# Kernel optimization log

Hardware: AMD Instinct MI355X
Metric: run time of the kernel (lower is better)

Reference implementation:

```python
import jax, jax.numpy as jnp
import numpy as np

N = 100000        # nodes
E = 1600000       # edges (avg degree 16)
D_IN = 128        # input feature dim
LAT = [32, 32, 32]
HID = 128
G = 1000          # graphs in batch


def _glorot(k, shape):
    lim = float(np.sqrt(6.0 / (shape[0] + shape[1])))
    return jax.random.uniform(k, shape, jnp.float32, -lim, lim)


def setup_inputs() -> dict:
    key = jax.random.key(0)
    ks = jax.random.split(key, 8)
    x = jax.random.normal(ks[0], (N, D_IN), jnp.float32)
    edge_index = jax.random.randint(ks[1], (2, E), 0, N, jnp.int32)
    # sorted graph assignment, every graph non-empty
    batch = ((jnp.arange(N, dtype=jnp.int32) * G) // N).astype(jnp.int32)
    W1 = _glorot(ks[2], (D_IN, LAT[0]));  b1 = jnp.zeros((LAT[0],), jnp.float32)
    W2 = _glorot(ks[3], (LAT[0], LAT[1])); b2 = jnp.zeros((LAT[1],), jnp.float32)
    W3 = _glorot(ks[4], (LAT[1], LAT[2])); b3 = jnp.zeros((LAT[2],), jnp.float32)
    lin1_w = _glorot(ks[5], (sum(LAT), HID)); lin1_b = jnp.zeros((HID,), jnp.float32)
    lin2_w = _glorot(ks[6], (HID, 2));        lin2_b = jnp.zeros((2,), jnp.float32)
    return dict(x=x, edge_index=edge_index, batch=batch, num_graphs=G,
                W1=W1, b1=b1, W2=W2, b2=b2, W3=W3, b3=b3,
                lin1_w=lin1_w, lin1_b=lin1_b, lin2_w=lin2_w, lin2_b=lin2_b)


def reference(x, edge_index, batch, num_graphs,
              W1, b1, W2, b2, W3, b3, lin1_w, lin1_b, lin2_w, lin2_b):
    n = x.shape[0]
    src, dst = edge_index[0], edge_index[1]
    # GCN sym-normalization with self-loops: deg[i] = 1 + in-degree(i)
    deg = jnp.ones((n,), x.dtype).at[dst].add(1.0)
    dis = jax.lax.rsqrt(deg)                      # deg^{-1/2}
    coef = (dis[src] * dis[dst])[:, None]         # [E,1] edge norm
    self_coef = (dis * dis)[:, None]              # [N,1] self-loop norm

    def gcn(h, W, b):
        h = h @ W                                  # transform first (PyG order)
        agg = jax.ops.segment_sum(h[src] * coef, dst, num_segments=n)
        return agg + h * self_coef + b

    h1 = jnp.tanh(gcn(x,  W1, b1))
    h2 = jnp.tanh(gcn(h1, W2, b2))
    h3 = jnp.tanh(gcn(h2, W3, b3))
    cat = jnp.concatenate([h1, h2, h3], axis=1)    # [N, 96]
    # readout: first node of each graph (batch is sorted)
    idx = jnp.searchsorted(batch, jnp.arange(num_graphs, dtype=batch.dtype))
    g = cat[idx]                                   # [G, 96]
    hidden = jax.nn.relu(g @ lin1_w + lin1_b)
    logits = jax.nn.log_softmax(hidden @ lin2_w + lin2_b, axis=1)
    return logits
```

## Files before the change

kernel.cpp:

```cpp
#include <hip/hip_runtime.h>
#include <math.h>


typedef int      int4v   __attribute__((ext_vector_type(4)));
typedef float    float4v __attribute__((ext_vector_type(4)));
typedef _Float16 half4v  __attribute__((ext_vector_type(4)));

#define NBLK 256
#define SB   500
#define CAPE 10240

__global__ void k_hist(const int* __restrict__ dst, int* __restrict__ blk_hist,
                       int E, int NP) {
    __shared__ int h[256];
    for (int i = threadIdx.x; i < NP; i += 256) h[i] = 0;
    __syncthreads();
    const int4v* d4 = (const int4v*)dst;
    int nv = E >> 2;
    int stride = gridDim.x * blockDim.x;
    for (int i = blockIdx.x * blockDim.x + threadIdx.x; i < nv; i += stride) {
        int4v d = __builtin_nontemporal_load(&d4[i]);
#pragma unroll
        for (int j = 0; j < 4; ++j) atomicAdd(&h[d[j] / SB], 1);
    }
    if (blockIdx.x == 0) {
        for (int e = (nv << 2) + threadIdx.x; e < E; e += blockDim.x)
            atomicAdd(&h[dst[e] / SB], 1);
    }
    __syncthreads();
    for (int i = threadIdx.x; i < NP; i += 256)
        blk_hist[blockIdx.x * NP + i] = h[i];
}

__global__ void k_total(const int* __restrict__ blk_hist, int* __restrict__ total, int NP) {
    __shared__ int s[256];
    int f = blockIdx.x;
    int acc = 0;
    for (int b = threadIdx.x; b < NBLK; b += 256) acc += blk_hist[b * NP + f];
    s[threadIdx.x] = acc;
    __syncthreads();
    for (int off = 128; off > 0; off >>= 1) {
        if (threadIdx.x < off) s[threadIdx.x] += s[threadIdx.x + off];
        __syncthreads();
    }
    if (threadIdx.x == 0) total[f] = s[0];
}

__global__ void k_sbase(const int* __restrict__ total, int* __restrict__ sbase, int NP) {
    __shared__ int s[256];
    int t = threadIdx.x;
    int v = (t < NP) ? total[t] : 0;
    s[t] = v;
    __syncthreads();
    for (int off = 1; off < 256; off <<= 1) {
        int u = (t >= off) ? s[t - off] : 0;
        __syncthreads();
        s[t] += u;
        __syncthreads();
    }
    if (t < NP) sbase[t] = s[t] - v;
    if (t == NP - 1) sbase[NP] = s[t];
}

__global__ void k_binoff(const int* __restrict__ blk_hist, const int* __restrict__ sbase,
                         int* __restrict__ blk_off, int NP) {
    __shared__ int s[NBLK];
    int f = blockIdx.x;
    int b = threadIdx.x;
    int v = blk_hist[b * NP + f];
    s[b] = v;
    __syncthreads();
    for (int off = 1; off < NBLK; off <<= 1) {
        int u = (b >= off) ? s[b - off] : 0;
        __syncthreads();
        s[b] += u;
        __syncthreads();
    }
    blk_off[b * NP + f] = sbase[f] + s[b] - v;
}

__global__ void k_split(const int* __restrict__ src, const int* __restrict__ dst,
                        const int* __restrict__ blk_off, uint2* __restrict__ pairs,
                        int E, int NP) {
    __shared__ int goff[256];
    for (int f = threadIdx.x; f < NP; f += 256)
        goff[f] = blk_off[blockIdx.x * NP + f];
    __syncthreads();
    const int4v* d4 = (const int4v*)dst;
    const int4v* s4 = (const int4v*)src;
    int nv = E >> 2;
    int stride = gridDim.x * blockDim.x;
    for (int i = blockIdx.x * blockDim.x + threadIdx.x; i < nv; i += stride) {
        int4v d = __builtin_nontemporal_load(&d4[i]);
        int4v s = __builtin_nontemporal_load(&s4[i]);
#pragma unroll
        for (int j = 0; j < 4; ++j) {
            int f = d[j] / SB;
            int pos = atomicAdd(&goff[f], 1);
            pairs[pos] = make_uint2((unsigned)s[j], (unsigned)d[j]);
        }
    }
    if (blockIdx.x == 0) {
        for (int e = (nv << 2) + threadIdx.x; e < E; e += blockDim.x) {
            int f = dst[e] / SB;
            int pos = atomicAdd(&goff[f], 1);
            pairs[pos] = make_uint2((unsigned)src[e], (unsigned)dst[e]);
        }
    }
}

__global__ void __launch_bounds__(512)
k_place(const uint2* __restrict__ pairs, const int* __restrict__ sbase,
        int* __restrict__ rowptr, float* __restrict__ dis,
        int* __restrict__ csr_src, int N, int NP) {
    __shared__ int lcnt[SB];
    __shared__ int lrp[SB + 1];
    __shared__ int sc[512];
    __shared__ int stage[CAPE];
    int f = blockIdx.x;
    int lo = f * SB;
    if (lo >= N) return;
    int hi = lo + SB; if (hi > N) hi = N;
    int sbc = hi - lo;
    int p0 = sbase[f], p1 = sbase[f + 1];
    int base = p0;
    int tid = threadIdx.x;
    for (int i = tid; i < sbc; i += 512) lcnt[i] = 0;
    __syncthreads();
    {
        int i = p0 + tid;
        for (; i + 3 * 512 < p1; i += 4 * 512) {
            uint2 a = pairs[i], c = pairs[i + 512], d = pairs[i + 1024], e = pairs[i + 1536];
            unsigned la = a.y - lo, lc = c.y - lo, ld = d.y - lo, le = e.y - lo;
            if (la < (unsigned)sbc) atomicAdd(&lcnt[la], 1);
            if (lc < (unsigned)sbc) atomicAdd(&lcnt[lc], 1);
            if (ld < (unsigned)sbc) atomicAdd(&lcnt[ld], 1);
            if (le < (unsigned)sbc) atomicAdd(&lcnt[le], 1);
        }
        for (; i < p1; i += 512) {
            unsigned ly = pairs[i].y - lo;
            if (ly < (unsigned)sbc) atomicAdd(&lcnt[ly], 1);
        }
    }
    __syncthreads();
    for (int i = tid; i < sbc; i += 512) dis[lo + i] = rsqrtf(1.0f + (float)lcnt[i]);
    int v = (tid < sbc) ? lcnt[tid] : 0;
    sc[tid] = v;
    __syncthreads();
    for (int off = 1; off < 512; off <<= 1) {
        int u = (tid >= off) ? sc[tid - off] : 0;
        __syncthreads();
        sc[tid] += u;
        __syncthreads();
    }
    if (tid < sbc) lrp[tid] = sc[tid] - v;
    if (tid == 511) lrp[sbc] = sc[511];
    __syncthreads();
    int T = lrp[sbc];
    for (int i = tid; i < sbc; i += 512) rowptr[lo + i] = base + lrp[i];
    if (hi == N && tid == 0) rowptr[N] = base + T;
    for (int i = tid; i < sbc; i += 512) lcnt[i] = 0;
    __syncthreads();
    {
        int i = p0 + tid;
        for (; i + 3 * 512 < p1; i += 4 * 512) {
            uint2 a = pairs[i], c = pairs[i + 512], d = pairs[i + 1024], e = pairs[i + 1536];
#pragma unroll
            for (int j = 0; j < 4; ++j) {
                uint2 p = (j == 0) ? a : (j == 1) ? c : (j == 2) ? d : e;
                unsigned ly = p.y - lo;
                if (ly < (unsigned)sbc) {
                    int slot = lrp[ly] + atomicAdd(&lcnt[ly], 1);
                    if (T <= CAPE) stage[slot] = (int)p.x;
                    else           csr_src[base + slot] = (int)p.x;
                }
            }
        }
        for (; i < p1; i += 512) {
            uint2 p = pairs[i];
            unsigned ly = p.y - lo;
            if (ly < (unsigned)sbc) {
                int slot = lrp[ly] + atomicAdd(&lcnt[ly], 1);
                if (T <= CAPE) stage[slot] = (int)p.x;
                else           csr_src[base + slot] = (int)p.x;
            }
        }
    }
    __syncthreads();
    if (T <= CAPE)
        for (int j = tid; j < T; j += 512) csr_src[base + j] = stage[j];
}

__global__ void k_gemm1(const float* __restrict__ h, const float* __restrict__ W,
                        const float* __restrict__ dis, _Float16* __restrict__ hps, int n) {
    __shared__ float sW[128 * 32];
    __shared__ float sh[64 * 132];
    int tid = threadIdx.x;
    int row0 = blockIdx.x * 64;
    for (int j = tid; j < 1024; j += 128)
        *(float4*)&sW[j * 4] = *(const float4*)&W[j * 4];
    for (int j = tid; j < 2048; j += 128) {
        int r = j >> 5, c4 = j & 31;
        float4v v = {0.f, 0.f, 0.f, 0.f};
        if (row0 + r < n)
            v = __builtin_nontemporal_load((const float4v*)&h[(size_t)(row0 + r) * 128 + c4 * 4]);
        *(float4v*)&sh[r * 132 + c4 * 4] = v;
    }
    __syncthreads();
    int rg = tid >> 3;
    int cg = tid & 7;
    float acc[4][4] = {};
    const float* shp = &sh[(rg * 4) * 132];
    const float* swp = &sW[cg * 4];
#pragma unroll 8
    for (int k4 = 0; k4 < 32; ++k4) {
        float4 hv[4], wv[4];
#pragma unroll
        for (int r = 0; r < 4; ++r) hv[r] = *(const float4*)&shp[r * 132 + k4 * 4];
#pragma unroll
        for (int t = 0; t < 4; ++t) wv[t] = *(const float4*)&swp[(k4 * 4 + t) * 32];
#pragma unroll
        for (int r = 0; r < 4; ++r) {
            const float hr[4] = {hv[r].x, hv[r].y, hv[r].z, hv[r].w};
#pragma unroll
            for (int t = 0; t < 4; ++t) {
                acc[r][0] += hr[t] * wv[t].x;
                acc[r][1] += hr[t] * wv[t].y;
                acc[r][2] += hr[t] * wv[t].z;
                acc[r][3] += hr[t] * wv[t].w;
            }
        }
    }
#pragma unroll
    for (int r = 0; r < 4; ++r) {
        int row = row0 + rg * 4 + r;
        if (row < n) {
            float dv = dis[row];
            half4v o = { (_Float16)(acc[r][0] * dv), (_Float16)(acc[r][1] * dv),
                         (_Float16)(acc[r][2] * dv), (_Float16)(acc[r][3] * dv) };
            *(half4v*)&hps[(size_t)row * 32 + cg * 4] = o;
        }
    }
}

template <bool FUSE>
__global__ void k_agg(const _Float16* __restrict__ hps, const int* __restrict__ rowptr,
                      const int* __restrict__ csr_src, const float* __restrict__ dis,
                      const float* __restrict__ bias, float* __restrict__ outc,
                      int n, const float* __restrict__ Wn, _Float16* __restrict__ hpsn) {
    __shared__ float sW[32 * 32];
    if (FUSE) {
        for (int i = threadIdx.x; i < 1024; i += 256) sW[i] = Wn[i];
        __syncthreads();
    }
    int g    = (blockIdx.x * blockDim.x + threadIdx.x) >> 5;
    int lane = threadIdx.x & 31;
    if (g >= n) return;
    float acc = (float)hps[(size_t)g * 32 + lane];
    int e0 = rowptr[g], e1 = rowptr[g + 1];
    int e = e0;
    while (e < e1) {
        int m = e1 - e; if (m > 32) m = 32;
        int sv = (e + lane < e1) ? __builtin_nontemporal_load(&csr_src[e + lane]) : 0;
        int k = 0;
        for (; k + 8 <= m; k += 8) {
            float v[8];
#pragma unroll
            for (int j = 0; j < 8; ++j) {
                int s = __shfl(sv, k + j, 32);
                v[j] = (float)hps[(size_t)s * 32 + lane];
            }
            acc += ((v[0] + v[1]) + (v[2] + v[3])) + ((v[4] + v[5]) + (v[6] + v[7]));
        }
        if (k + 4 <= m) {
            float v[4];
#pragma unroll
            for (int j = 0; j < 4; ++j) {
                int s = __shfl(sv, k + j, 32);
                v[j] = (float)hps[(size_t)s * 32 + lane];
            }
            acc += (v[0] + v[1]) + (v[2] + v[3]);
            k += 4;
        }
        for (; k < m; ++k) {
            int s = __shfl(sv, k, 32);
            acc += (float)hps[(size_t)s * 32 + lane];
        }
        e += m;
    }
    float dg = dis[g];
    float v = tanhf(dg * acc + bias[lane]);
    __builtin_nontemporal_store(v, &outc[(size_t)g * 96 + lane]);
    if (FUSE) {
        float a2 = 0.0f;
#pragma unroll
        for (int k = 0; k < 32; ++k)
            a2 += __shfl(v, k, 32) * sW[k * 32 + lane];
        hpsn[(size_t)g * 32 + lane] = (_Float16)(dg * a2);
    }
}

__global__ void k_idx(const int* __restrict__ batch, int* __restrict__ idx, int n, int g) {
    int i = blockIdx.x * blockDim.x + threadIdx.x;
    if (i >= g) return;
    int lo = 0, hi = n;
    while (lo < hi) {
        int mid = (lo + hi) >> 1;
        if (batch[mid] < i) lo = mid + 1; else hi = mid;
    }
    idx[i] = lo;
}

__global__ void k_head(const float* __restrict__ cat, const int* __restrict__ idx,
                       const float* __restrict__ w1, const float* __restrict__ b1,
                       const float* __restrict__ w2, const float* __restrict__ b2,
                       float* __restrict__ out) {
    __shared__ float gv[96];
    __shared__ float s0[128];
    __shared__ float s1[128];
    int g = blockIdx.x, t = threadIdx.x;
    int node = idx[g];
    if (t < 96) gv[t] = cat[(size_t)node * 96 + t];
    __syncthreads();
    float acc = b1[t];
#pragma unroll 8
    for (int i = 0; i < 96; ++i) acc += gv[i] * w1[i * 128 + t];
    float h = fmaxf(acc, 0.0f);
    s0[t] = h * w2[t * 2 + 0];
    s1[t] = h * w2[t * 2 + 1];
    __syncthreads();
    for (int off = 64; off > 0; off >>= 1) {
        if (t < off) { s0[t] += s0[t + off]; s1[t] += s1[t + off]; }
        __syncthreads();
    }
    if (t == 0) {
        float l0 = s0[0] + b2[0];
        float l1 = s1[0] + b2[1];
        float m  = fmaxf(l0, l1);
        float lse = m + logf(expf(l0 - m) + expf(l1 - m));
        out[(size_t)g * 2 + 0] = l0 - lse;
        out[(size_t)g * 2 + 1] = l1 - lse;
    }
}

extern "C" void kernel_launch(void* const* d_in, const int* in_sizes, int n_in,
                              void* d_out, int out_size, void* d_ws, size_t ws_size,
                              hipStream_t stream) {
    const float* x    = (const float*)d_in[0];
    const int*   ei   = (const int*)d_in[1];
    const int*   batch= (const int*)d_in[2];
    const float* W1   = (const float*)d_in[4];
    const float* b1   = (const float*)d_in[5];
    const float* W2   = (const float*)d_in[6];
    const float* b2   = (const float*)d_in[7];
    const float* W3   = (const float*)d_in[8];
    const float* b3   = (const float*)d_in[9];
    const float* l1w  = (const float*)d_in[10];
    const float* l1b  = (const float*)d_in[11];
    const float* l2w  = (const float*)d_in[12];
    const float* l2b  = (const float*)d_in[13];
    float* out = (float*)d_out;

    const int N = in_sizes[0] / 128;
    const int E = in_sizes[1] / 2;
    const int G = out_size / 2;
    const int* src = ei;
    const int* dst = ei + E;

    const int NP = (N + SB - 1) / SB;

    char* w = (char*)d_ws;
    auto alloc = [&](size_t bytes) {
        char* p = w;
        w += (bytes + 255) & ~(size_t)255;
        return p;
    };
    float*    dis      = (float*)   alloc((size_t)N * 4);
    int*      rowptr   = (int*)     alloc((size_t)(N + 1) * 4);
    int*      csr_src  = (int*)     alloc((size_t)E * 4);
    int*      blk_hist = (int*)     alloc((size_t)NBLK * NP * 4);
    int*      total    = (int*)     alloc((size_t)NP * 4);
    int*      sbase    = (int*)     alloc((size_t)(NP + 1) * 4);
    int*      blk_off  = (int*)     alloc((size_t)NBLK * NP * 4);
    uint2*    pairs    = (uint2*)   alloc((size_t)E * 8);
    _Float16* hpsA     = (_Float16*)alloc((size_t)N * 32 * 2);
    _Float16* hpsB     = (_Float16*)alloc((size_t)N * 32 * 2);
    float*    catb     = (float*)   alloc((size_t)N * 96 * 4);
    int*      idx      = (int*)     alloc((size_t)G * 4);

    const int nodes_bl = (N * 32 + 255) / 256;
    const int gemm_bl  = (N + 63) / 64;

    k_hist  <<<NBLK, 256, 0, stream>>>(dst, blk_hist, E, NP);
    k_total <<<NP,   256, 0, stream>>>(blk_hist, total, NP);
    k_sbase <<<1,    256, 0, stream>>>(total, sbase, NP);
    k_binoff<<<NP,  NBLK, 0, stream>>>(blk_hist, sbase, blk_off, NP);
    k_split <<<NBLK, 256, 0, stream>>>(src, dst, blk_off, pairs, E, NP);
    k_place <<<NP,   512, 0, stream>>>(pairs, sbase, rowptr, dis, csr_src, N, NP);

    k_gemm1<<<gemm_bl, 128, 0, stream>>>(x, W1, dis, hpsA, N);
    k_agg<true ><<<nodes_bl, 256, 0, stream>>>(hpsA, rowptr, csr_src, dis, b1, catb + 0,  N, W2, hpsB);
    k_agg<true ><<<nodes_bl, 256, 0, stream>>>(hpsB, rowptr, csr_src, dis, b2, catb + 32, N, W3, hpsA);
    k_agg<false><<<nodes_bl, 256, 0, stream>>>(hpsA, rowptr, csr_src, dis, b3, catb + 64, N, nullptr, nullptr);

    k_idx<<<(G + 255) / 256, 256, 0, stream>>>(batch, idx, N, G);
    k_head<<<G, 128, 0, stream>>>(catb, idx, l1w, l1b, l2w, l2b, out);
}
```

Before: 228.4 us.

## Split features into 4-column slices and gather per-slice with thread-per-node aggregation

Stores the transformed node features as eight column-slices of four halves each, laid out slice-major. The aggregation kernel now assigns one thread per node per slice, with slices taken from blockIdx, replacing the wave-per-node shuffle-based gather. The idea is that each slice (N*8 bytes) fits in cache, so random neighbour gathers hit L2. The fused next-layer GEMM is split into a separate kernel that reads the sliced fp32 layer output. The cost is two extra kernel launches, an extra global write and read of the intermediate activations, and CSR indices are re-read once per slice (8x index traffic). The head kernel is updated to read the new layout.

```diff
diff --git a/kernel.cpp b/kernel.cpp
--- a/kernel.cpp
+++ b/kernel.cpp
@@ -9,6 +9,11 @@
 #define NBLK 256
 #define SB   500
 #define CAPE 10240
+
+__device__ inline float4v h2f(half4v h) {
+    float4v f = { (float)h[0], (float)h[1], (float)h[2], (float)h[3] };
+    return f;
+}
 
 __global__ void k_hist(const int* __restrict__ dst, int* __restrict__ blk_hist,
                        int E, int NP) {
@@ -192,7 +197,7 @@
 }
 
 __global__ void k_gemm1(const float* __restrict__ h, const float* __restrict__ W,
-                        const float* __restrict__ dis, _Float16* __restrict__ hps, int n) {
+                        const float* __restrict__ dis, _Float16* __restrict__ hs, int n) {
     __shared__ float sW[128 * 32];
     __shared__ float sh[64 * 132];
     int tid = threadIdx.x;
@@ -238,65 +243,67 @@
             float dv = dis[row];
             half4v o = { (_Float16)(acc[r][0] * dv), (_Float16)(acc[r][1] * dv),
                          (_Float16)(acc[r][2] * dv), (_Float16)(acc[r][3] * dv) };
-            *(half4v*)&hps[(size_t)row * 32 + cg * 4] = o;
-        }
-    }
-}
-
-template <bool FUSE>
-__global__ void k_agg(const _Float16* __restrict__ hps, const int* __restrict__ rowptr,
-                      const int* __restrict__ csr_src, const float* __restrict__ dis,
-                      const float* __restrict__ bias, float* __restrict__ outc,
-                      int n, const float* __restrict__ Wn, _Float16* __restrict__ hpsn) {
+            *(half4v*)&hs[((size_t)cg * n + row) * 4] = o;
+        }
+    }
+}
+
+__global__ void k_aggs(const _Float16* __restrict__ hs, const int* __restrict__ rowptr,
+                       const int* __restrict__ csr_src, const float* __restrict__ dis,
+                       const float* __restrict__ bias, float* __restrict__ catl, int N) {
+    int q = blockIdx.x & 7;
+    int g = (blockIdx.x >> 3) * blockDim.x + threadIdx.x;
+    if (g >= N) return;
+    const half4v* hq = (const half4v*)(hs + (size_t)q * N * 4);
+    float4v acc = h2f(hq[g]);
+    int e = rowptr[g], e1 = rowptr[g + 1];
+    for (; e + 4 <= e1; e += 4) {
+        int s0 = csr_src[e],     s1 = csr_src[e + 1];
+        int s2 = csr_src[e + 2], s3 = csr_src[e + 3];
+        half4v h0 = hq[s0], h1 = hq[s1], h2 = hq[s2], h3 = hq[s3];
+        acc += (h2f(h0) + h2f(h1)) + (h2f(h2) + h2f(h3));
+    }
+    for (; e < e1; ++e) acc += h2f(hq[csr_src[e]]);
+    float dg = dis[g];
+    float4v bb = *(const float4v*)&bias[q * 4];
+    float4v v;
+    v[0] = tanhf(dg * acc[0] + bb[0]);
+    v[1] = tanhf(dg * acc[1] + bb[1]);
+    v[2] = tanhf(dg * acc[2] + bb[2]);
+    v[3] = tanhf(dg * acc[3] + bb[3]);
+    *(float4v*)&catl[((size_t)q * N + g) * 4] = v;
+}
+
+__global__ void k_gemms(const float* __restrict__ catl, const float* __restrict__ W,
+                        const float* __restrict__ dis, _Float16* __restrict__ hout, int N) {
     __shared__ float sW[32 * 32];
-    if (FUSE) {
-        for (int i = threadIdx.x; i < 1024; i += 256) sW[i] = Wn[i];
-        __syncthreads();
-    }
-    int g    = (blockIdx.x * blockDim.x + threadIdx.x) >> 5;
-    int lane = threadIdx.x & 31;
-    if (g >= n) return;
-    float acc = (float)hps[(size_t)g * 32 + lane];
-    int e0 = rowptr[g], e1 = rowptr[g + 1];
-    int e = e0;
-    while (e < e1) {
-        int m = e1 - e; if (m > 32) m = 32;
-        int sv = (e + lane < e1) ? __builtin_nontemporal_load(&csr_src[e + lane]) : 0;
-        int k = 0;
-        for (; k + 8 <= m; k += 8) {
-            float v[8];
-#pragma unroll
-            for (int j = 0; j < 8; ++j) {
-                int s = __shfl(sv, k + j, 32);
-                v[j] = (float)hps[(size_t)s * 32 + lane];
-            }
-            acc += ((v[0] + v[1]) + (v[2] + v[3])) + ((v[4] + v[5]) + (v[6] + v[7]));
-        }
-        if (k + 4 <= m) {
-            float v[4];
-#pragma unroll
-            for (int j = 0; j < 4; ++j) {
-                int s = __shfl(sv, k + j, 32);
-                v[j] = (float)hps[(size_t)s * 32 + lane];
-            }
-            acc += (v[0] + v[1]) + (v[2] + v[3]);
-            k += 4;
-        }
-        for (; k < m; ++k) {
-            int s = __shfl(sv, k, 32);
-            acc += (float)hps[(size_t)s * 32 + lane];
-        }
-        e += m;
-    }
-    float dg = dis[g];
-    float v = tanhf(dg * acc + bias[lane]);
-    __builtin_nontemporal_store(v, &outc[(size_t)g * 96 + lane]);
-    if (FUSE) {
-        float a2 = 0.0f;
-#pragma unroll
-        for (int k = 0; k < 32; ++k)
-            a2 += __shfl(v, k, 32) * sW[k * 32 + lane];
-        hpsn[(size_t)g * 32 + lane] = (_Float16)(dg * a2);
+    __shared__ float sv[32][33];
+    int tid = threadIdx.x;
+    int g0 = blockIdx.x * 32;
+    for (int i = tid; i < 1024; i += 256) sW[i] = W[i];
+    {
+        int qq = tid >> 5, i = tid & 31;
+        int g = g0 + i;
+        float4v vv = {0.f, 0.f, 0.f, 0.f};
+        if (g < N) vv = *(const float4v*)&catl[((size_t)qq * N + g) * 4];
+        sv[i][qq * 4 + 0] = vv[0]; sv[i][qq * 4 + 1] = vv[1];
+        sv[i][qq * 4 + 2] = vv[2]; sv[i][qq * 4 + 3] = vv[3];
+    }
+    __syncthreads();
+    int r = tid >> 3, cg = tid & 7;
+    float a0 = 0.f, a1 = 0.f, a2 = 0.f, a3 = 0.f;
+#pragma unroll 8
+    for (int k = 0; k < 32; ++k) {
+        float hv = sv[r][k];
+        const float* wp = &sW[k * 32 + cg * 4];
+        a0 += hv * wp[0]; a1 += hv * wp[1]; a2 += hv * wp[2]; a3 += hv * wp[3];
+    }
+    int g = g0 + r;
+    if (g < N) {
+        float dv = dis[g];
+        half4v o = { (_Float16)(a0 * dv), (_Float16)(a1 * dv),
+                     (_Float16)(a2 * dv), (_Float16)(a3 * dv) };
+        *(half4v*)&hout[((size_t)cg * N + g) * 4] = o;
     }
 }
 
@@ -314,13 +321,16 @@
 __global__ void k_head(const float* __restrict__ cat, const int* __restrict__ idx,
                        const float* __restrict__ w1, const float* __restrict__ b1,
                        const float* __restrict__ w2, const float* __restrict__ b2,
-                       float* __restrict__ out) {
+                       float* __restrict__ out, int N) {
     __shared__ float gv[96];
     __shared__ float s0[128];
     __shared__ float s1[128];
     int g = blockIdx.x, t = threadIdx.x;
     int node = idx[g];
-    if (t < 96) gv[t] = cat[(size_t)node * 96 + t];
+    if (t < 96) {
+        int l = t >> 5, rem = t & 31, qq = rem >> 2, c = rem & 3;
+        gv[t] = cat[(((size_t)l * 8 + qq) * N + node) * 4 + c];
+    }
     __syncthreads();
     float acc = b1[t];
 #pragma unroll 8
@@ -383,13 +393,15 @@
     int*      sbase    = (int*)     alloc((size_t)(NP + 1) * 4);
     int*      blk_off  = (int*)     alloc((size_t)NBLK * NP * 4);
     uint2*    pairs    = (uint2*)   alloc((size_t)E * 8);
-    _Float16* hpsA     = (_Float16*)alloc((size_t)N * 32 * 2);
-    _Float16* hpsB     = (_Float16*)alloc((size_t)N * 32 * 2);
+    _Float16* hsA      = (_Float16*)alloc((size_t)N * 32 * 2);
+    _Float16* hsB      = (_Float16*)alloc((size_t)N * 32 * 2);
     float*    catb     = (float*)   alloc((size_t)N * 96 * 4);
     int*      idx      = (int*)     alloc((size_t)G * 4);
 
-    const int nodes_bl = (N * 32 + 255) / 256;
     const int gemm_bl  = (N + 63) / 64;
+    const int aggs_bl  = ((N + 255) / 256) * 8;
+    const int gemms_bl = (N + 31) / 32;
+    const size_t LSTRIDE = (size_t)N * 32;
 
     k_hist  <<<NBLK, 256, 0, stream>>>(dst, blk_hist, E, NP);
     k_total <<<NP,   256, 0, stream>>>(blk_hist, total, NP);
@@ -398,11 +410,13 @@
     k_split <<<NBLK, 256, 0, stream>>>(src, dst, blk_off, pairs, E, NP);
     k_place <<<NP,   512, 0, stream>>>(pairs, sbase, rowptr, dis, csr_src, N, NP);
 
-    k_gemm1<<<gemm_bl, 128, 0, stream>>>(x, W1, dis, hpsA, N);
-    k_agg<true ><<<nodes_bl, 256, 0, stream>>>(hpsA, rowptr, csr_src, dis, b1, catb + 0,  N, W2, hpsB);
-    k_agg<true ><<<nodes_bl, 256, 0, stream>>>(hpsB, rowptr, csr_src, dis, b2, catb + 32, N, W3, hpsA);
-    k_agg<false><<<nodes_bl, 256, 0, stream>>>(hpsA, rowptr, csr_src, dis, b3, catb + 64, N, nullptr, nullptr);
+    k_gemm1<<<gemm_bl, 128, 0, stream>>>(x, W1, dis, hsA, N);
+    k_aggs <<<aggs_bl, 256, 0, stream>>>(hsA, rowptr, csr_src, dis, b1, catb + 0 * LSTRIDE, N);
+    k_gemms<<<gemms_bl, 256, 0, stream>>>(catb + 0 * LSTRIDE, W2, dis, hsB, N);
+    k_aggs <<<aggs_bl, 256, 0, stream>>>(hsB, rowptr, csr_src, dis, b2, catb + 1 * LSTRIDE, N);
+    k_gemms<<<gemms_bl, 256, 0, stream>>>(catb + 1 * LSTRIDE, W3, dis, hsA, N);
+    k_aggs <<<aggs_bl, 256, 0, stream>>>(hsA, rowptr, csr_src, dis, b3, catb + 2 * LSTRIDE, N);
 
     k_idx<<<(G + 255) / 256, 256, 0, stream>>>(batch, idx, N, G);
-    k_head<<<G, 128, 0, stream>>>(catb, idx, l1w, l1b, l2w, l2b, out);
-}
+    k_head<<<G, 128, 0, stream>>>(catb, idx, l1w, l1b, l2w, l2b, out, N);
+}
```

Result: slower. 325.1 us (+42.3%).
